# Optimization experiments

Measured on AMD Instinct MI355X. Metric: run time of the kernel, lower is better.

## Reference

```python
import jax, jax.numpy as jnp
import numpy as np

ANCHORS = np.array([116., 90., 156., 198., 373., 326.], np.float32).reshape(1, 1, 1, 3, 2)
IGNORE_THRESH = 0.5
OBJ_SCALE = 5.0
NOOBJ_SCALE = 1.0
XYWH_SCALE = 1.0
CLASS_SCALE = 1.0
GRID_SCALE = 1.0


def setup_inputs() -> dict:
    key = jax.random.key(0)
    k1, k2, k3 = jax.random.split(key, 3)
    B, GH, GW, NET, T, C = 16, 64, 64, 1024, 100, 80
    input_image = jnp.zeros((B, NET, NET, 3), jnp.float32)  # only shape is used
    y_pred = jax.random.normal(k1, (B, GH, GW, 3 * (5 + C)), jnp.float32)
    y_true = jax.random.uniform(k2, (B, GH, GW, 3, 5 + C), jnp.float32)
    true_boxes = jax.random.uniform(k3, (B, 1, 1, 1, T, 4), jnp.float32)
    return {"input_image": input_image, "y_pred": y_pred, "y_true": y_true, "true_boxes": true_boxes}


def reference(input_image, y_pred, y_true, true_boxes):
    B, GH, GW = y_true.shape[:3]
    net_h, net_w = input_image.shape[1], input_image.shape[2]
    dtype = y_pred.dtype
    anchors = jnp.asarray(ANCHORS, dtype)  # [1,1,1,3,2]
    y_pred = y_pred.reshape(B, GH, GW, 3, -1)
    object_mask = y_true[..., 4:5]  # [B,GH,GW,3,1]
    grid_factor = jnp.array([GW, GH], dtype).reshape(1, 1, 1, 1, 2)
    net_factor = jnp.array([net_w, net_h], dtype).reshape(1, 1, 1, 1, 2)
    cx, cy = jnp.meshgrid(jnp.arange(GW, dtype=dtype), jnp.arange(GH, dtype=dtype))
    cell_grid = jnp.stack([cx, cy], -1)[None, :, :, None, :]  # [1,GH,GW,1,2]

    # adjust predictions
    pred_box_xy = cell_grid + jax.nn.sigmoid(y_pred[..., :2])
    pred_box_wh = y_pred[..., 2:4]
    pred_box_conf = jax.nn.sigmoid(y_pred[..., 4:5])
    pred_box_class = y_pred[..., 5:]

    # adjust ground truth
    true_box_xy = y_true[..., 0:2]
    true_box_wh = y_true[..., 2:4]
    true_box_class = jnp.argmax(y_true[..., 5:], axis=-1)  # [B,GH,GW,3]

    # broadcast IoU: each predicted box vs all true boxes
    true_xy = true_boxes[..., 0:2] / grid_factor  # [B,1,1,1,T,2]
    true_wh = true_boxes[..., 2:4] / net_factor
    true_half = true_wh / 2.0
    true_mins, true_maxes = true_xy - true_half, true_xy + true_half
    pred_xy = (pred_box_xy / grid_factor)[..., None, :]  # [B,GH,GW,3,1,2]
    pred_wh = (jnp.exp(pred_box_wh) * anchors / net_factor)[..., None, :]
    pred_half = pred_wh / 2.0
    pred_mins, pred_maxes = pred_xy - pred_half, pred_xy + pred_half
    inter_wh = jnp.maximum(jnp.minimum(pred_maxes, true_maxes) - jnp.maximum(pred_mins, true_mins), 0.0)
    inter_area = inter_wh[..., 0] * inter_wh[..., 1]  # [B,GH,GW,3,T]
    true_area = true_wh[..., 0] * true_wh[..., 1]
    pred_area = pred_wh[..., 0] * pred_wh[..., 1]
    iou = inter_area / (pred_area + true_area - inter_area)
    best_ious = jnp.max(iou, axis=4)
    conf_ignore_mask = (best_ious > IGNORE_THRESH).astype(dtype)[..., None]

    # post-warmup branch (batch_seen > warmup_batches)
    xywh_mask = object_mask

    wh_scale = jnp.exp(true_box_wh) * anchors / net_factor
    wh_scale = (2.0 - wh_scale[..., 0] * wh_scale[..., 1])[..., None]

    xy_delta = xywh_mask * (true_box_xy - pred_box_xy) * wh_scale * XYWH_SCALE
    wh_delta = xywh_mask * (true_box_wh - pred_box_wh) * wh_scale * XYWH_SCALE
    conf_delta = (0.0 - pred_box_conf) * NOOBJ_SCALE
    conf_delta = conf_delta + object_mask * (1.0 - pred_box_conf) * OBJ_SCALE
    conf_delta = conf_delta * (1.0 - (1.0 - object_mask) * conf_ignore_mask)
    log_p = jax.nn.log_softmax(pred_box_class, axis=-1)
    ce = -jnp.take_along_axis(log_p, true_box_class[..., None], axis=-1)  # [B,GH,GW,3,1]
    class_delta = object_mask * ce * CLASS_SCALE

    delta = jnp.concatenate([xy_delta, wh_delta, conf_delta, class_delta], axis=-1)  # [B,GH,GW,3,6]
    loss = jnp.sum(jnp.square(delta), axis=(1, 2, 3, 4))
    return loss * GRID_SCALE
```

## Files before the change

### kernel.cpp

```cpp
#include <hip/hip_runtime.h>


#define NT 100
#define CPB 12288
#define NTOT 196608
#define RPB 128
#define CR 64
#define ROW_DW 85
#define CHUNK_DW (CR * ROW_DW)
#define CHUNK_F4 (CHUNK_DW / 4)

typedef float f4 __attribute__((ext_vector_type(4)));

__device__ __forceinline__ float frcp(float x) { return __builtin_amdgcn_rcpf(x); }
__device__ __forceinline__ float fsig(float x) { return frcp(1.f + __expf(-x)); }

__global__ __launch_bounds__(256) void yolo_loss_kernel(
    const float* __restrict__ y_pred,
    const float* __restrict__ y_true,
    const float* __restrict__ true_boxes,
    float* __restrict__ out)
{
    __shared__ __align__(16) float sp[CHUNK_DW];
    __shared__ __align__(16) float st[CHUNK_DW];
    __shared__ f4 sbox[NT];
    __shared__ float swsum[4];

    const int tid = threadIdx.x;
    const int block_row0 = blockIdx.x * RPB;
    const int b = block_row0 / CPB;

    if (tid < NT) {
        const f4 tb = *(const f4*)(true_boxes + (size_t)b * NT * 4 + tid * 4);
        const float tx = tb.x * (1.f / 64.f),   ty = tb.y * (1.f / 64.f);
        const float tw = tb.z * (1.f / 1024.f), th = tb.w * (1.f / 1024.f);
        f4 r;
        r.x = tx - 0.5f * tw; r.y = ty - 0.5f * th;
        r.z = tx + 0.5f * tw; r.w = ty + 0.5f * th;
        sbox[tid] = r;
    }

    const int R = tid >> 2;
    const int q = tid & 3;

    auto gload = [&](int c, f4* va, f4* wa) {
        const size_t base = ((size_t)(block_row0 + c * CR) * ROW_DW) >> 2;
        const f4* gp = (const f4*)y_pred + base;
        const f4* gt = (const f4*)y_true + base;
#pragma unroll
        for (int i = 0; i < 6; ++i) {
            const int idx = tid + 256 * i;
            if (idx < CHUNK_F4) { va[i] = gp[idx]; wa[i] = gt[idx]; }
        }
    };
    auto sstore = [&](const f4* va, const f4* wa) {
        f4* dp = (f4*)sp; f4* dt = (f4*)st;
#pragma unroll
        for (int i = 0; i < 6; ++i) {
            const int idx = tid + 256 * i;
            if (idx < CHUNK_F4) { dp[idx] = va[i]; dt[idx] = wa[i]; }
        }
    };

    auto consume = [&](int c) -> float {
        const float* P = sp + R * ROW_DW;
        const float* T = st + R * ROW_DW;

        const int row = block_row0 + c * CR + R;
        const int rem = row - b * CPB;
        const int gy  = rem / 192;
        const int rr  = rem - gy * 192;
        const int gx  = rr / 3;
        const int a   = rr - gx * 3;
        const float aw = (a == 0) ? 116.f : ((a == 1) ? 156.f : 373.f);
        const float ah = (a == 0) ? 90.f  : ((a == 1) ? 198.f : 326.f);

        float hp[8], ht[8];
#pragma unroll
        for (int e = 0; e < 8; ++e) { hp[e] = P[e]; ht[e] = T[e]; }

        float ssum = 0.f, tmax = -1e30f, psel = 0.f;
        int jm = 1 << 20;
        if (q == 0) {
#pragma unroll
            for (int e = 5; e < 8; ++e) {
                const float pv = hp[e], tv = ht[e];
                ssum += __expf(pv);
                const bool g = tv > tmax;
                tmax = g ? tv : tmax; psel = g ? pv : psel; jm = g ? (e - 5) : jm;
            }
        }
#pragma unroll
        for (int k = 0; k < 4; ++k) {
            const int d0 = 8 + 4 * q + 16 * k;
#pragma unroll
            for (int e = 0; e < 4; ++e) {
                const float pv = P[d0 + e], tv = T[d0 + e];
                ssum += __expf(pv);
                const bool g = tv > tmax;
                tmax = g ? tv : tmax; psel = g ? pv : psel;
                jm = g ? (d0 + e - 5) : jm;
            }
        }
        if (q < 3) {
            const int d0 = 72 + 4 * q;
#pragma unroll
            for (int e = 0; e < 4; ++e) {
                const float pv = P[d0 + e], tv = T[d0 + e];
                ssum += __expf(pv);
                const bool g = tv > tmax;
                tmax = g ? tv : tmax; psel = g ? pv : psel;
                jm = g ? (d0 + e - 5) : jm;
            }
        } else {
            const float pv = P[84], tv = T[84];
            ssum += __expf(pv);
            const bool g = tv > tmax;
            tmax = g ? tv : tmax; psel = g ? pv : psel; jm = g ? 79 : jm;
        }
#pragma unroll
        for (int off = 1; off < 4; off <<= 1) {
            ssum += __shfl_xor(ssum, off, 64);
            const float otm = __shfl_xor(tmax, off, 64);
            const float ops = __shfl_xor(psel, off, 64);
            const int   ojm = __shfl_xor(jm, off, 64);
            const bool adopt = (otm > tmax) || (otm == tmax && ojm < jm);
            tmax = adopt ? otm : tmax; psel = adopt ? ops : psel; jm = adopt ? ojm : jm;
        }
        const float ce = __logf(ssum) - psel;

        const float predx = (float)gx + fsig(hp[0]);
        const float predy = (float)gy + fsig(hp[1]);
        const float conf  = fsig(hp[4]);
        const float pw  = __expf(hp[2]) * aw * (1.f / 1024.f);
        const float phh = __expf(hp[3]) * ah * (1.f / 1024.f);
        const float parea = pw * phh;
        const float px = predx * (1.f / 64.f), py = predy * (1.f / 64.f);
        const float pminx = px - 0.5f * pw,  pmaxx = px + 0.5f * pw;
        const float pminy = py - 0.5f * phh, pmaxy = py + 0.5f * phh;

        float best = 0.f;
#pragma unroll 5
        for (int k = 0; k < 25; ++k) {
            const f4 bx = sbox[q + 4 * k];
            float iw = fminf(pmaxx, bx.z) - fmaxf(pminx, bx.x);
            float ih = fminf(pmaxy, bx.w) - fmaxf(pminy, bx.y);
            iw = fmaxf(iw, 0.f); ih = fmaxf(ih, 0.f);
            const float inter = iw * ih;
            const float tarea = (bx.z - bx.x) * (bx.w - bx.y);
            best = fmaxf(best, inter * frcp(parea + tarea - inter));
        }
#pragma unroll
        for (int off = 1; off < 4; off <<= 1)
            best = fmaxf(best, __shfl_xor(best, off, 64));
        const float ignore = (best > 0.5f) ? 1.f : 0.f;

        const float wsx = __expf(ht[2]) * aw * (1.f / 1024.f);
        const float wsy = __expf(ht[3]) * ah * (1.f / 1024.f);
        const float ws  = 2.f - wsx * wsy;
        const float om  = ht[4];
        const float omws = om * ws;
        const float dx = omws * (ht[0] - predx);
        const float dy = omws * (ht[1] - predy);
        const float dw = omws * (ht[2] - hp[2]);
        const float dh = omws * (ht[3] - hp[3]);
        float dc = -conf + om * (1.f - conf) * 5.f;
        dc *= (1.f - (1.f - om) * ignore);
        const float dcl = om * ce;

        const float val = dx * dx + dy * dy + dw * dw + dh * dh + dc * dc + dcl * dcl;
        return (q == 0) ? val : 0.f;
    };

    f4 va[6], wa[6], vb[6], wb[6];
    gload(0, va, wa);
    sstore(va, wa);
    __syncthreads();

    gload(1, vb, wb);
    float acc = consume(0);
    __syncthreads();

    sstore(vb, wb);
    __syncthreads();
    acc += consume(1);

#pragma unroll
    for (int off = 32; off > 0; off >>= 1) acc += __shfl_down(acc, off, 64);
    if ((tid & 63) == 0) swsum[tid >> 6] = acc;
    __syncthreads();
    if (tid == 0) atomicAdd(out + b, swsum[0] + swsum[1] + swsum[2] + swsum[3]);
}

extern "C" void kernel_launch(void* const* d_in, const int* in_sizes, int n_in,
                              void* d_out, int out_size, void* d_ws, size_t ws_size,
                              hipStream_t stream) {
    const float* y_pred     = (const float*)d_in[1];
    const float* y_true     = (const float*)d_in[2];
    const float* true_boxes = (const float*)d_in[3];
    float* out = (float*)d_out;

    hipMemsetAsync(d_out, 0, (size_t)out_size * sizeof(float), stream);
    yolo_loss_kernel<<<NTOT / RPB, 256, 0, stream>>>(y_pred, y_true, true_boxes, out);
}
```

Measured before the change: 326.1 us.

## Give each wave a private LDS chunk with register-prefetched pipeline, drop block barriers

Each wave now stages its own 16-row chunks in a private LDS slice and loops over 4 chunks. It prefetches the next chunk's global loads into registers while computing the current one, synchronising only at wave level instead of with block-wide __syncthreads. Blocks cover 256 rows instead of 128, which halves the grid and the number of atomics. The risks are fewer blocks in flight, a hand-written waitcnt that leaves the vmem count unbounded, and the safety of reusing LDS within a wave without a barrier.

```diff
diff --git a/kernel.cpp b/kernel.cpp
--- a/kernel.cpp
+++ b/kernel.cpp
@@ -4,11 +4,12 @@
 #define NT 100
 #define CPB 12288
 #define NTOT 196608
-#define RPB 128
-#define CR 64
+#define RPB 256
+#define CROWS 16
+#define NCH 4
 #define ROW_DW 85
-#define CHUNK_DW (CR * ROW_DW)
-#define CHUNK_F4 (CHUNK_DW / 4)
+#define CH_DW (CROWS * ROW_DW)
+#define CH_F4 (CH_DW / 4)
 
 typedef float f4 __attribute__((ext_vector_type(4)));
 
@@ -21,14 +22,19 @@
     const float* __restrict__ true_boxes,
     float* __restrict__ out)
 {
-    __shared__ __align__(16) float sp[CHUNK_DW];
-    __shared__ __align__(16) float st[CHUNK_DW];
+    __shared__ __align__(16) float slds[4][2 * CH_DW];
     __shared__ f4 sbox[NT];
     __shared__ float swsum[4];
 
-    const int tid = threadIdx.x;
+    const int tid  = threadIdx.x;
+    const int widx = tid >> 6;
+    const int lane = tid & 63;
+    const int R    = lane >> 2;
+    const int q    = lane & 3;
+
     const int block_row0 = blockIdx.x * RPB;
     const int b = block_row0 / CPB;
+    const int wave_row0 = block_row0 + widx * (CROWS * NCH);
 
     if (tid < NT) {
         const f4 tb = *(const f4*)(true_boxes + (size_t)b * NT * 4 + tid * 4);
@@ -39,34 +45,42 @@
         r.z = tx + 0.5f * tw; r.w = ty + 0.5f * th;
         sbox[tid] = r;
     }
-
-    const int R = tid >> 2;
-    const int q = tid & 3;
-
-    auto gload = [&](int c, f4* va, f4* wa) {
-        const size_t base = ((size_t)(block_row0 + c * CR) * ROW_DW) >> 2;
+    __syncthreads();
+
+    float* SW = slds[widx];
+
+    f4 va[6], wa[6];
+    auto gload = [&](int c) {
+        const size_t base = ((size_t)(wave_row0 + c * CROWS) * ROW_DW) >> 2;
         const f4* gp = (const f4*)y_pred + base;
         const f4* gt = (const f4*)y_true + base;
 #pragma unroll
-        for (int i = 0; i < 6; ++i) {
-            const int idx = tid + 256 * i;
-            if (idx < CHUNK_F4) { va[i] = gp[idx]; wa[i] = gt[idx]; }
-        }
+        for (int i = 0; i < 5; ++i) { va[i] = gp[lane + 64 * i]; }
+#pragma unroll
+        for (int i = 0; i < 5; ++i) { wa[i] = gt[lane + 64 * i]; }
+        if (lane < CH_F4 - 320) { va[5] = gp[lane + 320]; wa[5] = gt[lane + 320]; }
     };
-    auto sstore = [&](const f4* va, const f4* wa) {
-        f4* dp = (f4*)sp; f4* dt = (f4*)st;
-#pragma unroll
-        for (int i = 0; i < 6; ++i) {
-            const int idx = tid + 256 * i;
-            if (idx < CHUNK_F4) { dp[idx] = va[i]; dt[idx] = wa[i]; }
-        }
+    auto sstore = [&]() {
+        f4* dp = (f4*)SW;
+        f4* dt = dp + CH_F4;
+#pragma unroll
+        for (int i = 0; i < 5; ++i) { dp[lane + 64 * i] = va[i]; dt[lane + 64 * i] = wa[i]; }
+        if (lane < CH_F4 - 320) { dp[lane + 320] = va[5]; dt[lane + 320] = wa[5]; }
     };
 
-    auto consume = [&](int c) -> float {
-        const float* P = sp + R * ROW_DW;
-        const float* T = st + R * ROW_DW;
-
-        const int row = block_row0 + c * CR + R;
+    float acc = 0.f;
+    gload(0);
+    for (int c = 0; c < NCH; ++c) {
+        sstore();
+        if (c + 1 < NCH) gload(c + 1);
+
+        __builtin_amdgcn_s_waitcnt(0xC07F);
+        __builtin_amdgcn_wave_barrier();
+
+        const float* P = SW + R * ROW_DW;
+        const float* T = P + CH_DW;
+
+        const int row = wave_row0 + c * CROWS + R;
         const int rem = row - b * CPB;
         const int gy  = rem / 192;
         const int rr  = rem - gy * 192;
@@ -169,25 +183,12 @@
         const float dcl = om * ce;
 
         const float val = dx * dx + dy * dy + dw * dw + dh * dh + dc * dc + dcl * dcl;
-        return (q == 0) ? val : 0.f;
-    };
-
-    f4 va[6], wa[6], vb[6], wb[6];
-    gload(0, va, wa);
-    sstore(va, wa);
-    __syncthreads();
-
-    gload(1, vb, wb);
-    float acc = consume(0);
-    __syncthreads();
-
-    sstore(vb, wb);
-    __syncthreads();
-    acc += consume(1);
+        acc += (q == 0) ? val : 0.f;
+    }
 
 #pragma unroll
     for (int off = 32; off > 0; off >>= 1) acc += __shfl_down(acc, off, 64);
-    if ((tid & 63) == 0) swsum[tid >> 6] = acc;
+    if (lane == 0) swsum[widx] = acc;
     __syncthreads();
     if (tid == 0) atomicAdd(out + b, swsum[0] + swsum[1] + swsum[2] + swsum[3]);
 }
```

Measured after the change: 314.9 us. 3.4% less time.
